# Kernel optimization log

Measured on AMD Instinct MI355X. Metric: run time of the kernel, lower is better.

Reference implementation:

```python
import jax, jax.numpy as jnp
import numpy as np

B, T = 128, 50
VOCAB, EMB_D, GRU_H = 10000, 200, 100
HEADS, AHID, THID = 8, 96, 96

def _conv(x, w, b, pad):
    y = jax.lax.conv_general_dilated(x, w, (1, 1), pad,
        dimension_numbers=('NCHW', 'OIHW', 'NCHW'))
    return y + b[None, :, None, None]

def _bn(x, g, b, m, v):
    s = jax.lax.rsqrt(v + 1e-5)
    return (x - m[None, :, None, None]) * (g * s)[None, :, None, None] + b[None, :, None, None]

def _maxpool(x):
    return jax.lax.reduce_window(x, -jnp.inf, jax.lax.max, (1, 1, 2, 2), (1, 1, 2, 2), 'VALID')

def _resize(x):
    # F.interpolate(mode='bilinear', align_corners=False) == half-pixel bilinear, no antialias
    return jax.image.resize(x, (x.shape[0], x.shape[1], 25, 156), 'bilinear', antialias=False)

def _audio_attn(x, wq, bq, wk, bk, wv, bv):
    # x: [B,96,H,W]; wq: [heads,96,96] == stacked per-head 1x1 convs
    Q = jnp.einsum('bchw,noc->bnohw', x, wq) + bq[None, :, :, None, None]
    K = jnp.einsum('bchw,noc->bnohw', x, wk) + bk[None, :, :, None, None]
    V = jnp.einsum('bchw,noc->bnohw', x, wv) + bv[None, :, :, None, None]
    # torch F.softmax with no dim on a 4D tensor defaults to dim=1 (channels) -> axis=2 here
    return jax.nn.softmax(Q * K, axis=2) * V  # [B,heads,96,H,W]

def _text_attn(o, wq, bq, wk, bk, wv, bv):
    # o: [N,100]; wq: [heads,96,100] == stacked per-head Linear layers
    Q = jnp.einsum('nd,hod->nho', o, wq) + bq[None]
    K = jnp.einsum('nd,hod->nho', o, wk) + bk[None]
    V = jnp.einsum('nd,hod->nho', o, wv) + bv[None]
    a = jax.nn.softmax(Q * K, axis=2) * V  # 2D softmax default dim=1 -> over feature axis
    return a.reshape(o.shape[0], -1)  # head-concat order == torch cat along dim=1

def _gru(xs, w_ih, w_hh, b_ih, b_hh):
    # xs: [T,B,200]; torch gate order r, z, n; b_hn applied inside r-gating
    def step(h, x):
        gi = x @ w_ih.T + b_ih
        gh = h @ w_hh.T + b_hh
        ir, iz, inew = jnp.split(gi, 3, axis=1)
        hr, hz, hnew = jnp.split(gh, 3, axis=1)
        r = jax.nn.sigmoid(ir + hr)
        z = jax.nn.sigmoid(iz + hz)
        n = jnp.tanh(inew + r * hnew)
        h2 = (1.0 - z) * n + z * h
        return h2, h2
    h0 = jnp.zeros((xs.shape[1], GRU_H), xs.dtype)
    hT, outs = jax.lax.scan(step, h0, xs)
    return outs, hT

def _forward(tokens, lengths, mfcc_t, mfcc_f, mfcc_c, w1a, b1a, g1a, be1a, m1a, v1a, w1b, b1b, g1b, be1b, m1b, v1b, w2, b2, g2, be2, m2, v2, w3, b3, g3, be3, m3, v3, w4, b4, g4, be4, m4, v4, wq_a1, bq_a1, wk_a1, bk_a1, wv_a1, bv_a1, wq_a2, bq_a2, wk_a2, bk_a2, wv_a2, bv_a2, emb, w_ih, w_hh, b_ih, b_hh, wq_t1, bq_t1, wk_t1, bk_t1, wv_t1, bv_t1, wq_t2, bq_t2, wk_t2, bk_t2, wv_t2, bv_t2, w_fa, b_fa, w_ft, b_ft, w_e, b_e):
    # --- audio CNN stem (eval-mode batchnorm; dropout off) ---
    xa = jax.nn.relu(_bn(_conv(mfcc_t, w1a, b1a, 'VALID'), g1a, be1a, m1a, v1a))
    xb = jax.nn.relu(_bn(_conv(mfcc_f, w1b, b1b, 'VALID'), g1b, be1b, m1b, v1b))
    # NOTE: original source reuses conv1b/bn1b for the third input (faithful to that)
    xc = jax.nn.relu(_bn(_conv(mfcc_c, w1b, b1b, 'VALID'), g1b, be1b, m1b, v1b))
    x = jnp.concatenate([_resize(xa), _resize(xb), _resize(xc)], axis=1)  # [B,24,25,156]
    x = _maxpool(jax.nn.relu(_bn(_conv(x, w2, b2, [(1, 1), (1, 1)]), g2, be2, m2, v2)))  # [B,32,12,78]
    x = _maxpool(jax.nn.relu(_bn(_conv(x, w3, b3, [(1, 1), (1, 1)]), g3, be3, m3, v3)))  # [B,64,6,39]
    x = jax.nn.relu(_bn(_conv(x, w4, b4, [(1, 1), (1, 1)]), g4, be4, m4, v4))            # [B,96,6,39]
    # --- two stacked per-head audio attentions, then per-head spatial GAP ---
    a1 = _audio_attn(x, wq_a1, bq_a1, wk_a1, bk_a1, wv_a1, bv_a1).mean(axis=(-2, -1))  # [B,8,96]
    a2 = _audio_attn(x, wq_a2, bq_a2, wk_a2, bk_a2, wv_a2, bv_a2).mean(axis=(-2, -1))
    # forward() slices heads along the height concat and GAPs -> per head [stage1 96, stage2 96]
    self_attn_audio = jnp.concatenate([a1, a2], axis=2).reshape(x.shape[0], -1)  # [B,1536]
    # --- text branch: embedding + GRU (all lengths == T -> pack/pad is identity) ---
    ex = jnp.swapaxes(emb[tokens], 0, 1)  # [T,B,200]
    outs, h = _gru(ex, w_ih, w_hh, b_ih, b_hh)  # h: [B,100]
    output = jnp.swapaxes(outs, 0, 1).reshape(-1, GRU_H)  # [B*T,100]
    t1 = _text_attn(output, wq_t1, bq_t1, wk_t1, bk_t1, wv_t1, bv_t1)
    t2 = _text_attn(output, wq_t2, bq_t2, wk_t2, bk_t2, wv_t2, bv_t2)
    self_attn_text = jnp.concatenate([t1, t2], axis=1).reshape(x.shape[0], T, -1).sum(axis=1)  # [B,1536]
    # --- cross-modal gated fusion ---
    x_gap = x.mean(axis=(-2, -1))  # [B,96]
    a_text = jax.nn.softmax(x_gap @ w_fa.T + b_fa, axis=1)   # [B,100]
    attn_text_based_audio = a_text * h                        # [B,100]
    a_audio = jax.nn.softmax(h @ w_ft.T + b_ft, axis=1)      # [B,96]
    attn_audio_based_text = a_audio * x_gap                   # [B,96]
    feat = jnp.concatenate([self_attn_audio, self_attn_text,
                            attn_audio_based_text, attn_text_based_audio], axis=1)  # [B,3268]
    return feat @ w_e.T + b_e  # [B,4] emotion logits

def setup_inputs() -> dict:
    key = jax.random.key(0)
    ks = iter(jax.random.split(key, 100))
    nrm = lambda s, sc=0.05: jax.random.normal(next(ks), s, jnp.float32) * sc
    uni = lambda s: jax.random.uniform(next(ks), s, jnp.float32) * 0.5 + 0.5
    d = {}
    d['mfcc_t'] = jax.random.normal(next(ks), (B, 1, 200, 40), jnp.float32)
    d['mfcc_f'] = jax.random.normal(next(ks), (B, 1, 200, 40), jnp.float32)
    d['mfcc_c'] = jax.random.normal(next(ks), (B, 1, 200, 40), jnp.float32)
    d['tokens'] = jax.random.randint(next(ks), (B, T), 0, VOCAB)
    d['lengths'] = jnp.full((B,), T, jnp.int32)
    def bnp(pre, c):
        d['g' + pre] = 1.0 + nrm((c,)); d['be' + pre] = nrm((c,))
        d['m' + pre] = nrm((c,)); d['v' + pre] = uni((c,))
    d['w1a'] = nrm((8, 1, 5, 2), 0.2); d['b1a'] = nrm((8,)); bnp('1a', 8)
    d['w1b'] = nrm((8, 1, 2, 6), 0.2); d['b1b'] = nrm((8,)); bnp('1b', 8)
    d['w2'] = nrm((32, 24, 3, 3), 0.1); d['b2'] = nrm((32,)); bnp('2', 32)
    d['w3'] = nrm((64, 32, 3, 3), 0.1); d['b3'] = nrm((64,)); bnp('3', 64)
    d['w4'] = nrm((96, 64, 3, 3), 0.08); d['b4'] = nrm((96,)); bnp('4', 96)
    for s in ('1', '2'):
        for p in ('q', 'k', 'v'):
            d['w%s_a%s' % (p, s)] = nrm((HEADS, 96, 96), 0.1)
            d['b%s_a%s' % (p, s)] = nrm((HEADS, 96))
    d['emb'] = nrm((VOCAB, EMB_D), 0.1)
    d['w_ih'] = nrm((3 * GRU_H, EMB_D), 0.1); d['w_hh'] = nrm((3 * GRU_H, GRU_H), 0.1)
    d['b_ih'] = nrm((3 * GRU_H,)); d['b_hh'] = nrm((3 * GRU_H,))
    for s in ('1', '2'):
        for p in ('q', 'k', 'v'):
            d['w%s_t%s' % (p, s)] = nrm((HEADS, THID, GRU_H), 0.1)
            d['b%s_t%s' % (p, s)] = nrm((HEADS, THID))
    d['w_fa'] = nrm((100, 96), 0.1); d['b_fa'] = nrm((100,))
    d['w_ft'] = nrm((96, 100), 0.1); d['b_ft'] = nrm((96,))
    d['w_e'] = nrm((4, 2 * HEADS * AHID + 2 * HEADS * THID + 96 + 100), 0.05); d['b_e'] = nrm((4,))
    return d

def reference(mfcc_t, mfcc_f, mfcc_c, tokens, lengths, w1a, b1a, g1a, be1a, m1a, v1a, w1b, b1b, g1b, be1b, m1b, v1b, w2, b2, g2, be2, m2, v2, w3, b3, g3, be3, m3, v3, w4, b4, g4, be4, m4, v4, wq_a1, bq_a1, wk_a1, bk_a1, wv_a1, bv_a1, wq_a2, bq_a2, wk_a2, bk_a2, wv_a2, bv_a2, emb, w_ih, w_hh, b_ih, b_hh, wq_t1, bq_t1, wk_t1, bk_t1, wv_t1, bv_t1, wq_t2, bq_t2, wk_t2, bk_t2, wv_t2, bv_t2, w_fa, b_fa, w_ft, b_ft, w_e, b_e):
    return _forward(tokens, lengths, mfcc_t, mfcc_f, mfcc_c, w1a, b1a, g1a, be1a, m1a, v1a, w1b, b1b, g1b, be1b, m1b, v1b, w2, b2, g2, be2, m2, v2, w3, b3, g3, be3, m3, v3, w4, b4, g4, be4, m4, v4, wq_a1, bq_a1, wk_a1, bk_a1, wv_a1, bv_a1, wq_a2, bq_a2, wk_a2, bk_a2, wv_a2, bv_a2, emb, w_ih, w_hh, b_ih, b_hh, wq_t1, bq_t1, wk_t1, bk_t1, wv_t1, bv_t1, wq_t2, bq_t2, wk_t2, bk_t2, wv_t2, bv_t2, w_fa, b_fa, w_ft, b_ft, w_e, b_e)
```

## Files before the change

### kernel.cpp

```cpp
#include <hip/hip_runtime.h>
#include <math.h>

static constexpr int kB = 128;
static constexpr int kT = 50;

struct TDesc { const float* src; float* dst; int O; int C; int total; };
struct TPack { TDesc d[15]; };
__global__ void k_transpose_pack(TPack p) {
    TDesc t = p.d[blockIdx.y];
    int idx = blockIdx.x * 256 + threadIdx.x;
    if (idx >= t.total) return;
    int o = idx % t.O; int r = idx / t.O; int c = r % t.C; int n = r / t.C;
    t.dst[idx] = t.src[((size_t)n * t.O + o) * t.C + c];
}

__global__ void k_zero(float* __restrict__ a, int n) {
    int i = blockIdx.x * 256 + threadIdx.x;
    if (i < n) a[i] = 0.f;
}

__global__ void k_stem(const float* __restrict__ mt, const float* __restrict__ mf,
                       const float* __restrict__ mc,
                       const float* __restrict__ w1a, const float* __restrict__ b1a,
                       const float* __restrict__ g1a, const float* __restrict__ be1a,
                       const float* __restrict__ m1a, const float* __restrict__ v1a,
                       const float* __restrict__ w1b, const float* __restrict__ b1b,
                       const float* __restrict__ g1b, const float* __restrict__ be1b,
                       const float* __restrict__ m1b, const float* __restrict__ v1b,
                       float* __restrict__ out, int total) {
    int idx = blockIdx.x * blockDim.x + threadIdx.x;
    if (idx >= total) return;
    int ox = idx % 156; int t = idx / 156;
    int oy = t % 25; t /= 25;
    int ch = t % 24; int b = t / 24;
    int grp = ch >> 3, c = ch & 7;
    const float* src; int Hc, Wc;
    const float *wb, *cb, *g, *be, *m, *v;
    if (grp == 0) { src = mt; Hc = 196; Wc = 39; wb = w1a + c * 10;
                    cb = b1a; g = g1a; be = be1a; m = m1a; v = v1a; }
    else          { src = (grp == 1 ? mf : mc); Hc = 199; Wc = 35; wb = w1b + c * 12;
                    cb = b1b; g = g1b; be = be1b; m = m1b; v = v1b; }
    float s = g[c] * rsqrtf(v[c] + 1e-5f);
    float bias = (cb[c] - m[c]) * s + be[c];
    float sy = (oy + 0.5f) * ((float)Hc / 25.f) - 0.5f;
    float sx = (ox + 0.5f) * ((float)Wc / 156.f) - 0.5f;
    float fy0 = floorf(sy), fx0 = floorf(sx);
    float fy = sy - fy0, fx = sx - fx0;
    int y0 = (int)fy0, x0 = (int)fx0;
    int y0c = min(max(y0, 0), Hc - 1), y1c = min(max(y0 + 1, 0), Hc - 1);
    int x0c = min(max(x0, 0), Wc - 1), x1c = min(max(x0 + 1, 0), Wc - 1);
    bool xs = (x1c == x0c), ys = (y1c == y0c);
    const float* p = src + (size_t)b * 8000;
    float t00, t01, t10, t11;
    if (grp == 0) {
        float W[6][3];
        #pragma unroll
        for (int r = 0; r < 6; ++r) {
            int rr = min(y0c + r, 199);
            #pragma unroll
            for (int cc = 0; cc < 3; ++cc)
                W[r][cc] = p[rr * 40 + min(x0c + cc, 39)];
        }
        float a00 = 0.f, a01 = 0.f, a10 = 0.f, a11 = 0.f;
        #pragma unroll
        for (int ky = 0; ky < 5; ++ky)
            #pragma unroll
            for (int kx = 0; kx < 2; ++kx) {
                float wv = wb[ky * 2 + kx];
                a00 += W[ky][kx] * wv;     a01 += W[ky][kx + 1] * wv;
                a10 += W[ky + 1][kx] * wv; a11 += W[ky + 1][kx + 1] * wv;
            }
        t00 = a00;
        t01 = xs ? a00 : a01;
        t10 = ys ? a00 : a10;
        t11 = xs ? (ys ? a00 : a10) : (ys ? a01 : a11);
    } else {
        float W[3][7];
        #pragma unroll
        for (int r = 0; r < 3; ++r) {
            int rr = min(y0c + r, 199);
            #pragma unroll
            for (int cc = 0; cc < 7; ++cc)
                W[r][cc] = p[rr * 40 + min(x0c + cc, 39)];
        }
        float a00 = 0.f, a01 = 0.f, a10 = 0.f, a11 = 0.f;
        #pragma unroll
        for (int ky = 0; ky < 2; ++ky)
            #pragma unroll
            for (int kx = 0; kx < 6; ++kx) {
                float wv = wb[ky * 6 + kx];
                a00 += W[ky][kx] * wv;     a01 += W[ky][kx + 1] * wv;
                a10 += W[ky + 1][kx] * wv; a11 += W[ky + 1][kx + 1] * wv;
            }
        t00 = a00;
        t01 = xs ? a00 : a01;
        t10 = ys ? a00 : a10;
        t11 = xs ? (ys ? a00 : a10) : (ys ? a01 : a11);
    }
    float r00 = fmaxf(t00 * s + bias, 0.f), r01 = fmaxf(t01 * s + bias, 0.f);
    float r10 = fmaxf(t10 * s + bias, 0.f), r11 = fmaxf(t11 * s + bias, 0.f);
    out[idx] = r00 * (1.f - fy) * (1.f - fx) + r01 * (1.f - fy) * fx
             + r10 * fy * (1.f - fx) + r11 * fy * fx;
}

template<int CIN, int CI_T, int H, int W, int ROWS, int NPX>
__global__ void __launch_bounds__(256) k_conv3x3_tiled(
    const float* __restrict__ in, const float* __restrict__ wT,
    const float* __restrict__ cb, const float* __restrict__ g,
    const float* __restrict__ be, const float* __restrict__ m,
    const float* __restrict__ v, float* __restrict__ out, int COUT) {
    constexpr int WP = W + 2;
    constexpr int RP = ROWS + 2;
    constexpr int STAGE = CI_T * RP * WP;
    __shared__ float sx[STAGE];
    __shared__ float sw[CI_T * 9 * 8];
    const int b = blockIdx.x, rt = blockIdx.y, oc0 = blockIdx.z * 8;
    const int row0 = rt * ROWS;
    const int tid = threadIdx.x;

    int off[NPX]; bool val[NPX];
    #pragma unroll
    for (int j = 0; j < NPX; ++j) {
        int px = tid + j * 256;
        int oy = px / W, ox = px - oy * W;
        bool ok = (px < ROWS * W) && (row0 + oy < H);
        val[j] = ok;
        off[j] = ok ? (oy * WP + ox) : 0;
    }

    float acc[NPX][8];
    #pragma unroll
    for (int j = 0; j < NPX; ++j)
        #pragma unroll
        for (int o = 0; o < 8; ++o) acc[j][o] = 0.f;

    for (int c0 = 0; c0 < CIN; c0 += CI_T) {
        __syncthreads();
        for (int e = tid; e < STAGE; e += 256) {
            int ci = e / (RP * WP);
            int rem = e - ci * RP * WP;
            int r = rem / WP;
            int xx = rem - r * WP;
            int iy = row0 - 1 + r;
            int ix = xx - 1;
            float vv = 0.f;
            if (iy >= 0 && iy < H && ix >= 0 && ix < W)
                vv = in[((size_t)(b * CIN + c0 + ci) * H + iy) * W + ix];
            sx[e] = vv;
        }
        for (int e = tid; e < CI_T * 9 * 8; e += 256) {
            int rk = e >> 3;
            int o = e & 7;
            sw[e] = wT[((size_t)c0 * 9 + rk) * COUT + oc0 + o];
        }
        __syncthreads();
        #pragma unroll 1
        for (int cl = 0; cl < CI_T; ++cl) {
            const float* sxc = sx + cl * RP * WP;
            #pragma unroll
            for (int k = 0; k < 9; ++k) {
                const int ky = k / 3, kx = k % 3;
                const float4 wa = *(const float4*)(sw + (cl * 9 + k) * 8);
                const float4 wb = *(const float4*)(sw + (cl * 9 + k) * 8 + 4);
                #pragma unroll
                for (int j = 0; j < NPX; ++j) {
                    float xv = sxc[off[j] + ky * WP + kx];
                    acc[j][0] += xv * wa.x; acc[j][1] += xv * wa.y;
                    acc[j][2] += xv * wa.z; acc[j][3] += xv * wa.w;
                    acc[j][4] += xv * wb.x; acc[j][5] += xv * wb.y;
                    acc[j][6] += xv * wb.z; acc[j][7] += xv * wb.w;
                }
            }
        }
    }
    float sc[8], bi[8];
    #pragma unroll
    for (int o = 0; o < 8; ++o) {
        float s = g[oc0 + o] * rsqrtf(v[oc0 + o] + 1e-5f);
        sc[o] = s; bi[o] = (cb[oc0 + o] - m[oc0 + o]) * s + be[oc0 + o];
    }
    #pragma unroll
    for (int j = 0; j < NPX; ++j) if (val[j]) {
        int px = tid + j * 256;
        int oy = row0 + px / W, ox = px % W;
        #pragma unroll
        for (int o = 0; o < 8; ++o)
            out[((size_t)(b * COUT + oc0 + o) * H + oy) * W + ox] =
                fmaxf(acc[j][o] * sc[o] + bi[o], 0.f);
    }
}

__global__ void k_maxpool(const float* __restrict__ in, float* __restrict__ out,
                          int C, int Hin, int Win, int Hout, int Wout, int total) {
    int idx = blockIdx.x * blockDim.x + threadIdx.x;
    if (idx >= total) return;
    int ox = idx % Wout; int t = idx / Wout;
    int oy = t % Hout; t /= Hout;
    int c = t % C; int b = t / C;
    const float* p = in + ((size_t)(b * C + c) * Hin + 2 * oy) * Win + 2 * ox;
    float m0 = fmaxf(p[0], p[1]);
    float m1 = fmaxf(p[Win], p[Win + 1]);
    out[idx] = fmaxf(m0, m1);
}

__global__ void __launch_bounds__(256) k_xgap(const float* __restrict__ x,
                                              float* __restrict__ xgap) {
    int b = blockIdx.x, tid = threadIdx.x;
    int wave = tid >> 6, lane = tid & 63;
    for (int c = wave; c < 96; c += 4) {
        const float* row = x + ((size_t)b * 96 + c) * 234;
        float s = 0.f;
        for (int p = lane; p < 234; p += 64) s += row[p];
        #pragma unroll
        for (int off = 1; off < 64; off <<= 1) s += __shfl_xor(s, off);
        if (lane == 0) xgap[b * 96 + c] = s * (1.f / 234.f);
    }
}

__global__ void __launch_bounds__(256, 2) k_audio_attn(
    const float* __restrict__ x,
    const float* __restrict__ wq1, const float* __restrict__ bq1,
    const float* __restrict__ wk1, const float* __restrict__ bk1,
    const float* __restrict__ wv1, const float* __restrict__ bv1,
    const float* __restrict__ wq2, const float* __restrict__ bq2,
    const float* __restrict__ wk2, const float* __restrict__ bk2,
    const float* __restrict__ wv2, const float* __restrict__ bv2,
    float* __restrict__ afeat) {
    const int b = blockIdx.x >> 1, pt = blockIdx.x & 1;
    const int n = blockIdx.y, stage = blockIdx.z;
    const float* wq = (stage ? wq2 : wq1) + n * 9216;
    const float* wk = (stage ? wk2 : wk1) + n * 9216;
    const float* wv = (stage ? wv2 : wv1) + n * 9216;
    const float* bqn = (stage ? bq2 : bq1) + n * 96;
    const float* bkn = (stage ? bk2 : bk1) + n * 96;
    const float* bvn = (stage ? bv2 : bv1) + n * 96;
    const int tid = threadIdx.x;
    const int to = tid >> 4, tpg = tid & 15;
    const int ob = to * 6;
    const int pA = tpg * 4;
    const int p0 = pt * 128;

    __shared__ float sxc[16 * 128];
    __shared__ float sw[4608];
    float* sred = sw;

    const float* xb = x + (size_t)b * (96 * 234) + p0;

    float qa[6][8], ka[6][8], va[6][8];
    #pragma unroll
    for (int j = 0; j < 6; ++j) {
        float bq_ = bqn[ob + j], bk_ = bkn[ob + j], bv_ = bvn[ob + j];
        #pragma unroll
        for (int i = 0; i < 8; ++i) { qa[j][i] = bq_; ka[j][i] = bk_; va[j][i] = bv_; }
    }

    for (int c0 = 0; c0 < 96; c0 += 16) {
        __syncthreads();
        {
            #pragma unroll
            for (int it = 0; it < 4; ++it) {
                int e2 = tid + it * 256;
                int r = e2 >> 6, c2 = (e2 & 63) * 2;
                float2 v = make_float2(0.f, 0.f);
                if (p0 + c2 < 234) v = *(const float2*)(xb + (c0 + r) * 234 + c2);
                *(float2*)(sxc + r * 128 + c2) = v;
            }
        }
        for (int e4 = tid; e4 < 1152; e4 += 256) {
            int mat = (e4 >= 768) ? 2 : (e4 >= 384 ? 1 : 0);
            int r4 = e4 - mat * 384;
            const float* wsrc = (mat == 0) ? wq : (mat == 1 ? wk : wv);
            *(float4*)(sw + mat * 1536 + r4 * 4) = *(const float4*)(wsrc + c0 * 96 + r4 * 4);
        }
        __syncthreads();
        #pragma unroll 2
        for (int cc = 0; cc < 16; ++cc) {
            float4 xa = *(const float4*)(sxc + cc * 128 + pA);
            float4 xc = *(const float4*)(sxc + cc * 128 + 64 + pA);
            const float* wr = sw + cc * 96 + ob;
            float2 q01 = *(const float2*)(wr);
            float2 q23 = *(const float2*)(wr + 2);
            float2 q45 = *(const float2*)(wr + 4);
            float2 k01 = *(const float2*)(wr + 1536);
            float2 k23 = *(const float2*)(wr + 1538);
            float2 k45 = *(const float2*)(wr + 1540);
            float2 v01 = *(const float2*)(wr + 3072);
            float2 v23 = *(const float2*)(wr + 3074);
            float2 v45 = *(const float2*)(wr + 3076);
            float wqv[6] = {q01.x, q01.y, q23.x, q23.y, q45.x, q45.y};
            float wkv[6] = {k01.x, k01.y, k23.x, k23.y, k45.x, k45.y};
            float wvv[6] = {v01.x, v01.y, v23.x, v23.y, v45.x, v45.y};
            #pragma unroll
            for (int j = 0; j < 6; ++j) {
                qa[j][0] += wqv[j] * xa.x; qa[j][1] += wqv[j] * xa.y;
                qa[j][2] += wqv[j] * xa.z; qa[j][3] += wqv[j] * xa.w;
                qa[j][4] += wqv[j] * xc.x; qa[j][5] += wqv[j] * xc.y;
                qa[j][6] += wqv[j] * xc.z; qa[j][7] += wqv[j] * xc.w;
                ka[j][0] += wkv[j] * xa.x; ka[j][1] += wkv[j] * xa.y;
                ka[j][2] += wkv[j] * xa.z; ka[j][3] += wkv[j] * xa.w;
                ka[j][4] += wkv[j] * xc.x; ka[j][5] += wkv[j] * xc.y;
                ka[j][6] += wkv[j] * xc.z; ka[j][7] += wkv[j] * xc.w;
                va[j][0] += wvv[j] * xa.x; va[j][1] += wvv[j] * xa.y;
                va[j][2] += wvv[j] * xa.z; va[j][3] += wvv[j] * xa.w;
                va[j][4] += wvv[j] * xc.x; va[j][5] += wvv[j] * xc.y;
                va[j][6] += wvv[j] * xc.z; va[j][7] += wvv[j] * xc.w;
            }
        }
    }

    int col[8];
    #pragma unroll
    for (int i = 0; i < 4; ++i) { col[i] = pA + i; col[4 + i] = 64 + pA + i; }

    float pmx[8];
    #pragma unroll
    for (int i = 0; i < 8; ++i) pmx[i] = -1e30f;
    #pragma unroll
    for (int j = 0; j < 6; ++j)
        #pragma unroll
        for (int i = 0; i < 8; ++i) {
            float sv = qa[j][i] * ka[j][i];
            qa[j][i] = sv;
            pmx[i] = fmaxf(pmx[i], sv);
        }
    __syncthreads();
    #pragma unroll
    for (int i = 0; i < 8; ++i) sred[to * 128 + col[i]] = pmx[i];
    __syncthreads();
    float m_[8];
    #pragma unroll
    for (int i = 0; i < 8; ++i) {
        float mm = -1e30f;
        for (int t = 0; t < 16; ++t) mm = fmaxf(mm, sred[t * 128 + col[i]]);
        m_[i] = mm;
    }
    __syncthreads();
    float z[8];
    #pragma unroll
    for (int i = 0; i < 8; ++i) z[i] = 0.f;
    #pragma unroll
    for (int j = 0; j < 6; ++j)
        #pragma unroll
        for (int i = 0; i < 8; ++i) {
            float e = __expf(qa[j][i] - m_[i]);
            qa[j][i] = e;
            z[i] += e;
        }
    #pragma unroll
    for (int i = 0; i < 8; ++i) sred[to * 128 + col[i]] = z[i];
    __syncthreads();
    float rz[8];
    #pragma unroll
    for (int i = 0; i < 8; ++i) {
        float zs = 0.f;
        for (int t = 0; t < 16; ++t) zs += sred[t * 128 + col[i]];
        rz[i] = (p0 + col[i] < 234) ? 1.f / zs : 0.f;
    }
    __syncthreads();
    #pragma unroll
    for (int j = 0; j < 6; ++j) {
        float po = 0.f;
        #pragma unroll
        for (int i = 0; i < 8; ++i) po += qa[j][i] * rz[i] * va[j][i];
        sred[(ob + j) * 16 + tpg] = po;
    }
    __syncthreads();
    if (tid < 96) {
        float ssum = 0.f;
        #pragma unroll
        for (int t = 0; t < 16; ++t) ssum += sred[tid * 16 + t];
        atomicAdd(afeat + b * 1536 + n * 192 + stage * 96 + tid, ssum * (1.f / 234.f));
    }
}

__global__ void __launch_bounds__(320) k_gi(const int* __restrict__ tokens,
        const float* __restrict__ emb, const float* __restrict__ w_ih,
        const float* __restrict__ b_ih, float* __restrict__ GI) {
    int r0 = blockIdx.x * 8;
    int tid = threadIdx.x;
    __shared__ float er[8][200];
    for (int e = tid; e < 1600; e += 320) {
        int r = e / 200, c = e - r * 200;
        er[r][c] = emb[(size_t)tokens[r0 + r] * 200 + c];
    }
    __syncthreads();
    if (tid < 300) {
        float acc[8];
        float bv = b_ih[tid];
        #pragma unroll
        for (int r = 0; r < 8; ++r) acc[r] = bv;
        for (int k4 = 0; k4 < 50; ++k4) {
            float4 w4 = *(const float4*)(w_ih + (size_t)tid * 200 + k4 * 4);
            #pragma unroll
            for (int r = 0; r < 8; ++r) {
                float4 x4 = *(const float4*)&er[r][k4 * 4];
                acc[r] += w4.x * x4.x + w4.y * x4.y + w4.z * x4.z + w4.w * x4.w;
            }
        }
        #pragma unroll
        for (int r = 0; r < 8; ++r)
            GI[(size_t)(r0 + r) * 300 + tid] = acc[r];
    }
}

__global__ void __launch_bounds__(320) k_gru_all(const float* __restrict__ GI,
        const float* __restrict__ w_hh, const float* __restrict__ b_hh,
        float* __restrict__ outs) {
    int b = blockIdx.x, tid = threadIdx.x;
    __shared__ float hs[100];
    __shared__ float gH[300];
    float4 wreg[25];
    float bias = 0.f;
    if (tid < 300) {
        bias = b_hh[tid];
        #pragma unroll
        for (int k4 = 0; k4 < 25; ++k4)
            wreg[k4] = *(const float4*)(w_hh + (size_t)tid * 100 + k4 * 4);
    }
    if (tid < 100) hs[tid] = 0.f;
    __syncthreads();
    for (int t = 0; t < kT; ++t) {
        if (tid < 300) {
            float gh = bias;
            #pragma unroll
            for (int k4 = 0; k4 < 25; ++k4) {
                float4 h4 = *(const float4*)&hs[k4 * 4];
                gh += wreg[k4].x * h4.x + wreg[k4].y * h4.y
                    + wreg[k4].z * h4.z + wreg[k4].w * h4.w;
            }
            gH[tid] = gh;
        }
        __syncthreads();
        if (tid < 100) {
            const float* gi = GI + ((size_t)b * kT + t) * 300;
            float r = 1.f / (1.f + expf(-(gi[tid] + gH[tid])));
            float z = 1.f / (1.f + expf(-(gi[100 + tid] + gH[100 + tid])));
            float nn = tanhf(gi[200 + tid] + r * gH[200 + tid]);
            float h2 = (1.f - z) * nn + z * hs[tid];
            hs[tid] = h2;
            outs[((size_t)b * kT + t) * 100 + tid] = h2;
        }
        __syncthreads();
    }
}

__global__ void __launch_bounds__(128) k_text_attn(const float* __restrict__ outs,
    const float* __restrict__ wq1, const float* __restrict__ bq1,
    const float* __restrict__ wk1, const float* __restrict__ bk1,
    const float* __restrict__ wv1, const float* __restrict__ bv1,
    const float* __restrict__ wq2, const float* __restrict__ bq2,
    const float* __restrict__ wk2, const float* __restrict__ bk2,
    const float* __restrict__ wv2, const float* __restrict__ bv2,
    float* __restrict__ tfeat) {
    int b = blockIdx.x, stage = blockIdx.y, n = blockIdx.z;
    const float* wq = stage ? wq2 : wq1; const float* bq = stage ? bq2 : bq1;
    const float* wk = stage ? wk2 : wk1; const float* bk = stage ? bk2 : bk1;
    const float* wv = stage ? wv2 : wv1; const float* bv = stage ? bv2 : bv1;
    int tid = threadIdx.x;
    bool act = tid < 96;
    int oo = act ? tid : 0;
    const float* wqc = wq + n * 9600 + oo;
    const float* wkc = wk + n * 9600 + oo;
    const float* wvc = wv + n * 9600 + oo;
    float bqv = act ? bq[n * 96 + tid] : 0.f;
    float bkv = act ? bk[n * 96 + tid] : 0.f;
    float bvv = act ? bv[n * 96 + tid] : 0.f;
    __shared__ float rows[10][100];
    __shared__ float wredM[2][10], wredS[2][10];
    float acc = 0.f;
    int wave = tid >> 6, lane = tid & 63;
    for (int tile = 0; tile < 5; ++tile) {
        int t0 = tile * 10;
        __syncthreads();
        for (int e = tid; e < 1000; e += 128) {
            int tt = e / 100, c = e - tt * 100;
            rows[tt][c] = outs[((size_t)b * kT + t0 + tt) * 100 + c];
        }
        __syncthreads();
        float q[10], k[10], v[10];
        #pragma unroll
        for (int tt = 0; tt < 10; ++tt) { q[tt] = bqv; k[tt] = bkv; v[tt] = bvv; }
        for (int c4 = 0; c4 < 25; ++c4) {
            int cb = c4 * 4 * 96;
            float q0 = wqc[cb], q1 = wqc[cb + 96], q2 = wqc[cb + 192], q3 = wqc[cb + 288];
            float k0 = wkc[cb], k1 = wkc[cb + 96], k2 = wkc[cb + 192], k3 = wkc[cb + 288];
            float v0 = wvc[cb], v1 = wvc[cb + 96], v2 = wvc[cb + 192], v3 = wvc[cb + 288];
            #pragma unroll
            for (int tt = 0; tt < 10; ++tt) {
                float4 x4 = *(const float4*)&rows[tt][c4 * 4];
                q[tt] += q0 * x4.x + q1 * x4.y + q2 * x4.z + q3 * x4.w;
                k[tt] += k0 * x4.x + k1 * x4.y + k2 * x4.z + k3 * x4.w;
                v[tt] += v0 * x4.x + v1 * x4.y + v2 * x4.z + v3 * x4.w;
            }
        }
        float s[10], e_[10];
        #pragma unroll
        for (int tt = 0; tt < 10; ++tt) s[tt] = act ? q[tt] * k[tt] : -1e30f;
        #pragma unroll
        for (int tt = 0; tt < 10; ++tt) {
            float m = s[tt];
            #pragma unroll
            for (int off = 1; off < 64; off <<= 1) m = fmaxf(m, __shfl_xor(m, off));
            if (lane == 0) wredM[wave][tt] = m;
        }
        __syncthreads();
        #pragma unroll
        for (int tt = 0; tt < 10; ++tt) {
            float mx = fmaxf(wredM[0][tt], wredM[1][tt]);
            e_[tt] = expf(s[tt] - mx);
        }
        #pragma unroll
        for (int tt = 0; tt < 10; ++tt) {
            float sm = e_[tt];
            #pragma unroll
            for (int off = 1; off < 64; off <<= 1) sm += __shfl_xor(sm, off);
            if (lane == 0) wredS[wave][tt] = sm;
        }
        __syncthreads();
        #pragma unroll
        for (int tt = 0; tt < 10; ++tt) {
            float sm = wredS[0][tt] + wredS[1][tt];
            acc += e_[tt] / sm * v[tt];
        }
    }
    if (act) tfeat[b * 1536 + stage * 768 + n * 96 + tid] = acc;
}

__global__ void __launch_bounds__(128) k_final(const float* __restrict__ xgap,
    const float* __restrict__ outs, const float* __restrict__ afeat,
    const float* __restrict__ tfeat,
    const float* __restrict__ w_fa, const float* __restrict__ b_fa,
    const float* __restrict__ w_ft, const float* __restrict__ b_ft,
    const float* __restrict__ w_e, const float* __restrict__ b_e,
    float* __restrict__ out) {
    int b = blockIdx.x; int tid = threadIdx.x;
    __shared__ float xg[96], hv[100], st[100], sa[96], aat[96], atba[100];
    __shared__ float redm[2], reds[2];
    if (tid < 96) xg[tid] = xgap[b * 96 + tid];
    if (tid < 100) hv[tid] = outs[(size_t)(b * kT + kT - 1) * 100 + tid];
    __syncthreads();
    if (tid < 100) {
        float acc = b_fa[tid];
        const float* wr = w_fa + tid * 96;
        for (int c = 0; c < 96; ++c) acc += wr[c] * xg[c];
        st[tid] = acc;
    }
    if (tid < 96) {
        float acc = b_ft[tid];
        const float* wr = w_ft + tid * 100;
        for (int c = 0; c < 100; ++c) acc += wr[c] * hv[c];
        sa[tid] = acc;
    }
    __syncthreads();
    if (tid == 0) {
        float mxv = -1e30f; for (int i = 0; i < 100; ++i) mxv = fmaxf(mxv, st[i]);
        float s = 0.f; for (int i = 0; i < 100; ++i) s += expf(st[i] - mxv);
        redm[0] = mxv; reds[0] = s;
    }
    if (tid == 1) {
        float mxv = -1e30f; for (int i = 0; i < 96; ++i) mxv = fmaxf(mxv, sa[i]);
        float s = 0.f; for (int i = 0; i < 96; ++i) s += expf(sa[i] - mxv);
        redm[1] = mxv; reds[1] = s;
    }
    __syncthreads();
    if (tid < 100) atba[tid] = expf(st[tid] - redm[0]) / reds[0] * hv[tid];
    if (tid < 96)  aat[tid]  = expf(sa[tid] - redm[1]) / reds[1] * xg[tid];
    __syncthreads();
    float a0 = 0.f, a1 = 0.f, a2 = 0.f, a3 = 0.f;
    for (int col = tid; col < 3268; col += 128) {
        float f;
        if (col < 1536)      f = afeat[b * 1536 + col];
        else if (col < 3072) f = tfeat[b * 1536 + col - 1536];
        else if (col < 3168) f = aat[col - 3072];
        else                 f = atba[col - 3168];
        a0 += w_e[col] * f;            a1 += w_e[3268 + col] * f;
        a2 += w_e[2 * 3268 + col] * f; a3 += w_e[3 * 3268 + col] * f;
    }
    __shared__ float r4[4][128];
    r4[0][tid] = a0; r4[1][tid] = a1; r4[2][tid] = a2; r4[3][tid] = a3;
    __syncthreads();
    if (tid < 4) {
        float s = 0.f;
        for (int i = 0; i < 128; ++i) s += r4[tid][i];
        out[b * 4 + tid] = s + b_e[tid];
    }
}

extern "C" void kernel_launch(void* const* d_in, const int* in_sizes, int n_in,
                              void* d_out, int out_size, void* d_ws, size_t ws_size,
                              hipStream_t stream) {
    (void)in_sizes; (void)n_in; (void)out_size; (void)ws_size;
    const float* mfcc_t = (const float*)d_in[0];
    const float* mfcc_f = (const float*)d_in[1];
    const float* mfcc_c = (const float*)d_in[2];
    const int*   tokens = (const int*)d_in[3];
    const float *w1a = (const float*)d_in[5],  *b1a = (const float*)d_in[6],
                *g1a = (const float*)d_in[7],  *be1a = (const float*)d_in[8],
                *m1a = (const float*)d_in[9],  *v1a = (const float*)d_in[10];
    const float *w1b = (const float*)d_in[11], *b1b = (const float*)d_in[12],
                *g1b = (const float*)d_in[13], *be1b = (const float*)d_in[14],
                *m1b = (const float*)d_in[15], *v1b = (const float*)d_in[16];
    const float *w2 = (const float*)d_in[17], *b2 = (const float*)d_in[18],
                *g2 = (const float*)d_in[19], *be2 = (const float*)d_in[20],
                *m2 = (const float*)d_in[21], *v2 = (const float*)d_in[22];
    const float *w3 = (const float*)d_in[23], *b3 = (const float*)d_in[24],
                *g3 = (const float*)d_in[25], *be3 = (const float*)d_in[26],
                *m3 = (const float*)d_in[27], *v3 = (const float*)d_in[28];
    const float *w4 = (const float*)d_in[29], *b4 = (const float*)d_in[30],
                *g4 = (const float*)d_in[31], *be4 = (const float*)d_in[32],
                *m4 = (const float*)d_in[33], *v4 = (const float*)d_in[34];
    const float *wq_a1 = (const float*)d_in[35], *bq_a1 = (const float*)d_in[36],
                *wk_a1 = (const float*)d_in[37], *bk_a1 = (const float*)d_in[38],
                *wv_a1 = (const float*)d_in[39], *bv_a1 = (const float*)d_in[40];
    const float *wq_a2 = (const float*)d_in[41], *bq_a2 = (const float*)d_in[42],
                *wk_a2 = (const float*)d_in[43], *bk_a2 = (const float*)d_in[44],
                *wv_a2 = (const float*)d_in[45], *bv_a2 = (const float*)d_in[46];
    const float *emb  = (const float*)d_in[47];
    const float *w_ih = (const float*)d_in[48], *w_hh = (const float*)d_in[49],
                *b_ih = (const float*)d_in[50], *b_hh = (const float*)d_in[51];
    const float *wq_t1 = (const float*)d_in[52], *bq_t1 = (const float*)d_in[53],
                *wk_t1 = (const float*)d_in[54], *bk_t1 = (const float*)d_in[55],
                *wv_t1 = (const float*)d_in[56], *bv_t1 = (const float*)d_in[57];
    const float *wq_t2 = (const float*)d_in[58], *bq_t2 = (const float*)d_in[59],
                *wk_t2 = (const float*)d_in[60], *bk_t2 = (const float*)d_in[61],
                *wv_t2 = (const float*)d_in[62], *bv_t2 = (const float*)d_in[63];
    const float *w_fa = (const float*)d_in[64], *b_fa = (const float*)d_in[65],
                *w_ft = (const float*)d_in[66], *b_ft = (const float*)d_in[67],
                *w_e  = (const float*)d_in[68], *b_e  = (const float*)d_in[69];

    float* ws = (float*)d_ws;
    const size_t Z0 = 0;
    const size_t Z1 = 22091776ull;
    const size_t OUTS  = 34072576ull;
    const size_t AFEAT = 34712576ull;
    const size_t TFEAT = 34909184ull;
    const size_t XGAP  = 35105792ull;
    const size_t WT    = 35118080ull;
    float* X1 = ws + Z1;
    float* C2 = ws + Z0;  float* P2 = ws + Z1;
    float* C3 = ws + Z0;  float* P3 = ws + Z1;
    float* X4 = ws + Z0;  float* GI = ws + Z1;
    float* outs  = ws + OUTS;
    float* afeat = ws + AFEAT;
    float* tfeat = ws + TFEAT;
    float* xgap  = ws + XGAP;
    float* wqa1t = ws + WT;
    float* wka1t = wqa1t + 73728; float* wva1t = wka1t + 73728;
    float* wqa2t = wva1t + 73728; float* wka2t = wqa2t + 73728; float* wva2t = wka2t + 73728;
    float* wqt1t = wva2t + 73728;
    float* wkt1t = wqt1t + 76800; float* wvt1t = wkt1t + 76800;
    float* wqt2t = wvt1t + 76800; float* wkt2t = wqt2t + 76800; float* wvt2t = wkt2t + 76800;
    float* wT2 = outs;
    float* wT3 = outs + 6912;
    float* wT4 = outs + 25344;

    TPack tp;
    tp.d[0]  = {wq_a1, wqa1t, 96, 96, 73728};
    tp.d[1]  = {wk_a1, wka1t, 96, 96, 73728};
    tp.d[2]  = {wv_a1, wva1t, 96, 96, 73728};
    tp.d[3]  = {wq_a2, wqa2t, 96, 96, 73728};
    tp.d[4]  = {wk_a2, wka2t, 96, 96, 73728};
    tp.d[5]  = {wv_a2, wva2t, 96, 96, 73728};
    tp.d[6]  = {w2, wT2, 32, 216, 6912};
    tp.d[7]  = {w3, wT3, 64, 288, 18432};
    tp.d[8]  = {w4, wT4, 96, 576, 55296};
    tp.d[9]  = {wq_t1, wqt1t, 96, 100, 76800};
    tp.d[10] = {wk_t1, wkt1t, 96, 100, 76800};
    tp.d[11] = {wv_t1, wvt1t, 96, 100, 76800};
    tp.d[12] = {wq_t2, wqt2t, 96, 100, 76800};
    tp.d[13] = {wk_t2, wkt2t, 96, 100, 76800};
    tp.d[14] = {wv_t2, wvt2t, 96, 100, 76800};
    k_transpose_pack<<<dim3(300, 15), 256, 0, stream>>>(tp);

    k_zero<<<768, 256, 0, stream>>>(afeat, 196608);

    k_stem<<<46800, 256, 0, stream>>>(mfcc_t, mfcc_f, mfcc_c,
        w1a, b1a, g1a, be1a, m1a, v1a,
        w1b, b1b, g1b, be1b, m1b, v1b, X1, 11980800);
    k_conv3x3_tiled<24, 8, 25, 156, 9, 6><<<dim3(128, 3, 4), 256, 0, stream>>>(
        X1, wT2, b2, g2, be2, m2, v2, C2, 32);
    k_maxpool<<<14976, 256, 0, stream>>>(C2, P2, 32, 25, 156, 12, 78, 3833856);
    k_conv3x3_tiled<32, 8, 12, 78, 12, 4><<<dim3(128, 1, 8), 256, 0, stream>>>(
        P2, wT3, b3, g3, be3, m3, v3, C3, 64);
    k_maxpool<<<7488, 256, 0, stream>>>(C3, P3, 64, 12, 78, 6, 39, 1916928);
    k_conv3x3_tiled<64, 16, 6, 39, 6, 1><<<dim3(128, 1, 12), 256, 0, stream>>>(
        P3, wT4, b4, g4, be4, m4, v4, X4, 96);

    k_xgap<<<kB, 256, 0, stream>>>(X4, xgap);

    k_audio_attn<<<dim3(kB * 2, 8, 2), 256, 0, stream>>>(X4,
        wqa1t, bq_a1, wka1t, bk_a1, wva1t, bv_a1,
        wqa2t, bq_a2, wka2t, bk_a2, wva2t, bv_a2, afeat);

    k_gi<<<kB * kT / 8, 320, 0, stream>>>(tokens, emb, w_ih, b_ih, GI);
    k_gru_all<<<kB, 320, 0, stream>>>(GI, w_hh, b_hh, outs);
    k_text_attn<<<dim3(kB, 2, 8), 128, 0, stream>>>(outs,
        wqt1t, bq_t1, wkt1t, bk_t1, wvt1t, bv_t1,
        wqt2t, bq_t2, wkt2t, bk_t2, wvt2t, bv_t2, tfeat);

    k_final<<<kB, 128, 0, stream>>>(xgap, outs, afeat, tfeat,
                                    w_fa, b_fa, w_ft, b_ft, w_e, b_e, (float*)d_out);
}
```

Baseline: 1.418 ms.

## Horizontally fuse independent kernels to overlap serial GRU with stem and attention

The afeat zeroing moves into the transpose-pack launch as an extra grid row. The GRU recurrence runs as 128 extra blocks inside the stem launch, so the serial 50-step loop overlaps with the bilinear stem. xgap, text attention and audio attention become one launch that selects its role from the block index. This cuts launch count and hides GRU latency, but the fused GRU now reads w_hh from global memory each step instead of keeping it in registers. Workspace aliases are rearranged (GI to Z0, conv weights to tfeat) so the concurrently running branches do not overlap in memory.

```diff
diff --git a/kernel.cpp b/kernel.cpp
--- a/kernel.cpp
+++ b/kernel.cpp
@@ -6,7 +6,12 @@
 
 struct TDesc { const float* src; float* dst; int O; int C; int total; };
 struct TPack { TDesc d[15]; };
-__global__ void k_transpose_pack(TPack p) {
+__global__ void k_transpose_pack(TPack p, float* __restrict__ za) {
+    if (blockIdx.y == 15) {
+        for (int i = blockIdx.x * 256 + threadIdx.x; i < 196608; i += 76800)
+            za[i] = 0.f;
+        return;
+    }
     TDesc t = p.d[blockIdx.y];
     int idx = blockIdx.x * 256 + threadIdx.x;
     if (idx >= t.total) return;
@@ -14,21 +19,94 @@
     t.dst[idx] = t.src[((size_t)n * t.O + o) * t.C + c];
 }
 
-__global__ void k_zero(float* __restrict__ a, int n) {
-    int i = blockIdx.x * 256 + threadIdx.x;
-    if (i < n) a[i] = 0.f;
+__global__ void __launch_bounds__(320) k_gi(const int* __restrict__ tokens,
+        const float* __restrict__ emb, const float* __restrict__ w_ih,
+        const float* __restrict__ b_ih, float* __restrict__ GI) {
+    int r0 = blockIdx.x * 8;
+    int tid = threadIdx.x;
+    __shared__ float er[8][200];
+    for (int e = tid; e < 1600; e += 320) {
+        int r = e / 200, c = e - r * 200;
+        er[r][c] = emb[(size_t)tokens[r0 + r] * 200 + c];
+    }
+    __syncthreads();
+    if (tid < 300) {
+        float acc[8];
+        float bv = b_ih[tid];
+        #pragma unroll
+        for (int r = 0; r < 8; ++r) acc[r] = bv;
+        for (int k4 = 0; k4 < 50; ++k4) {
+            float4 w4 = *(const float4*)(w_ih + (size_t)tid * 200 + k4 * 4);
+            #pragma unroll
+            for (int r = 0; r < 8; ++r) {
+                float4 x4 = *(const float4*)&er[r][k4 * 4];
+                acc[r] += w4.x * x4.x + w4.y * x4.y + w4.z * x4.z + w4.w * x4.w;
+            }
+        }
+        #pragma unroll
+        for (int r = 0; r < 8; ++r)
+            GI[(size_t)(r0 + r) * 300 + tid] = acc[r];
+    }
 }
 
-__global__ void k_stem(const float* __restrict__ mt, const float* __restrict__ mf,
-                       const float* __restrict__ mc,
-                       const float* __restrict__ w1a, const float* __restrict__ b1a,
-                       const float* __restrict__ g1a, const float* __restrict__ be1a,
-                       const float* __restrict__ m1a, const float* __restrict__ v1a,
-                       const float* __restrict__ w1b, const float* __restrict__ b1b,
-                       const float* __restrict__ g1b, const float* __restrict__ be1b,
-                       const float* __restrict__ m1b, const float* __restrict__ v1b,
-                       float* __restrict__ out, int total) {
-    int idx = blockIdx.x * blockDim.x + threadIdx.x;
+__global__ void __launch_bounds__(256) k_fat_stem_gru(
+    const float* __restrict__ mt, const float* __restrict__ mf,
+    const float* __restrict__ mc,
+    const float* __restrict__ w1a, const float* __restrict__ b1a,
+    const float* __restrict__ g1a, const float* __restrict__ be1a,
+    const float* __restrict__ m1a, const float* __restrict__ v1a,
+    const float* __restrict__ w1b, const float* __restrict__ b1b,
+    const float* __restrict__ g1b, const float* __restrict__ be1b,
+    const float* __restrict__ m1b, const float* __restrict__ v1b,
+    float* __restrict__ out, int total,
+    const float* __restrict__ GI, const float* __restrict__ w_hh,
+    const float* __restrict__ b_hh, float* __restrict__ outs) {
+    if (blockIdx.x < 128) {
+        const int b = blockIdx.x, tid = threadIdx.x;
+        __shared__ float hs[100];
+        __shared__ float gH[300];
+        const float bias0 = b_hh[tid];
+        const float bias1 = (tid < 44) ? b_hh[256 + tid] : 0.f;
+        if (tid < 100) hs[tid] = 0.f;
+        __syncthreads();
+        for (int t = 0; t < kT; ++t) {
+            {
+                float gh = bias0;
+                const float* wr = w_hh + (size_t)tid * 100;
+                #pragma unroll
+                for (int k4 = 0; k4 < 25; ++k4) {
+                    float4 w4 = *(const float4*)(wr + k4 * 4);
+                    float4 h4 = *(const float4*)&hs[k4 * 4];
+                    gh += w4.x * h4.x + w4.y * h4.y + w4.z * h4.z + w4.w * h4.w;
+                }
+                gH[tid] = gh;
+            }
+            if (tid < 44) {
+                float gh = bias1;
+                const float* wr = w_hh + (size_t)(256 + tid) * 100;
+                #pragma unroll
+                for (int k4 = 0; k4 < 25; ++k4) {
+                    float4 w4 = *(const float4*)(wr + k4 * 4);
+                    float4 h4 = *(const float4*)&hs[k4 * 4];
+                    gh += w4.x * h4.x + w4.y * h4.y + w4.z * h4.z + w4.w * h4.w;
+                }
+                gH[256 + tid] = gh;
+            }
+            __syncthreads();
+            if (tid < 100) {
+                const float* gi = GI + ((size_t)b * kT + t) * 300;
+                float r = 1.f / (1.f + expf(-(gi[tid] + gH[tid])));
+                float z = 1.f / (1.f + expf(-(gi[100 + tid] + gH[100 + tid])));
+                float nn = tanhf(gi[200 + tid] + r * gH[200 + tid]);
+                float h2 = (1.f - z) * nn + z * hs[tid];
+                hs[tid] = h2;
+                outs[((size_t)b * kT + t) * 100 + tid] = h2;
+            }
+            __syncthreads();
+        }
+        return;
+    }
+    int idx = (blockIdx.x - 128) * 256 + threadIdx.x;
     if (idx >= total) return;
     int ox = idx % 156; int t = idx / 156;
     int oy = t % 25; t /= 25;
@@ -203,21 +281,7 @@
     out[idx] = fmaxf(m0, m1);
 }
 
-__global__ void __launch_bounds__(256) k_xgap(const float* __restrict__ x,
-                                              float* __restrict__ xgap) {
-    int b = blockIdx.x, tid = threadIdx.x;
-    int wave = tid >> 6, lane = tid & 63;
-    for (int c = wave; c < 96; c += 4) {
-        const float* row = x + ((size_t)b * 96 + c) * 234;
-        float s = 0.f;
-        for (int p = lane; p < 234; p += 64) s += row[p];
-        #pragma unroll
-        for (int off = 1; off < 64; off <<= 1) s += __shfl_xor(s, off);
-        if (lane == 0) xgap[b * 96 + c] = s * (1.f / 234.f);
-    }
-}
-
-__global__ void __launch_bounds__(256, 2) k_audio_attn(
+__global__ void __launch_bounds__(256, 2) k_fat_attn(
     const float* __restrict__ x,
     const float* __restrict__ wq1, const float* __restrict__ bq1,
     const float* __restrict__ wk1, const float* __restrict__ bk1,
@@ -225,23 +289,127 @@
     const float* __restrict__ wq2, const float* __restrict__ bq2,
     const float* __restrict__ wk2, const float* __restrict__ bk2,
     const float* __restrict__ wv2, const float* __restrict__ bv2,
-    float* __restrict__ afeat) {
-    const int b = blockIdx.x >> 1, pt = blockIdx.x & 1;
-    const int n = blockIdx.y, stage = blockIdx.z;
+    float* __restrict__ afeat,
+    const float* __restrict__ outs,
+    const float* __restrict__ wqt1, const float* __restrict__ bqt1,
+    const float* __restrict__ wkt1, const float* __restrict__ bkt1,
+    const float* __restrict__ wvt1, const float* __restrict__ bvt1,
+    const float* __restrict__ wqt2, const float* __restrict__ bqt2,
+    const float* __restrict__ wkt2, const float* __restrict__ bkt2,
+    const float* __restrict__ wvt2, const float* __restrict__ bvt2,
+    float* __restrict__ tfeat, float* __restrict__ xgap) {
+    __shared__ float smem[6656];
+    const int bx = blockIdx.x;
+    const int tid = threadIdx.x;
+
+    if (bx >= 6144) {
+        int b = bx - 6144;
+        int wave = tid >> 6, lane = tid & 63;
+        for (int c = wave; c < 96; c += 4) {
+            const float* row = x + ((size_t)b * 96 + c) * 234;
+            float s = 0.f;
+            for (int p = lane; p < 234; p += 64) s += row[p];
+            #pragma unroll
+            for (int off = 1; off < 64; off <<= 1) s += __shfl_xor(s, off);
+            if (lane == 0) xgap[b * 96 + c] = s * (1.f / 234.f);
+        }
+        return;
+    }
+    if (bx >= 4096) {
+        int a = bx - 4096;
+        int b = a & 127, rem = a >> 7;
+        int stage = rem & 1, n = rem >> 1;
+        const float* wq = stage ? wqt2 : wqt1; const float* bq = stage ? bqt2 : bqt1;
+        const float* wk = stage ? wkt2 : wkt1; const float* bk = stage ? bkt2 : bkt1;
+        const float* wv = stage ? wvt2 : wvt1; const float* bv = stage ? bvt2 : bvt1;
+        bool act = tid < 96;
+        int oo = act ? tid : 0;
+        const float* wqc = wq + n * 9600 + oo;
+        const float* wkc = wk + n * 9600 + oo;
+        const float* wvc = wv + n * 9600 + oo;
+        float bqv = act ? bq[n * 96 + tid] : 0.f;
+        float bkv = act ? bk[n * 96 + tid] : 0.f;
+        float bvv = act ? bv[n * 96 + tid] : 0.f;
+        float* rows = smem;
+        float* wredM = smem + 1000;
+        float* wredS = smem + 1020;
+        float acc = 0.f;
+        int wave = tid >> 6, lane = tid & 63;
+        for (int tile = 0; tile < 5; ++tile) {
+            int t0 = tile * 10;
+            __syncthreads();
+            for (int e = tid; e < 1000; e += 256) {
+                int tt = e / 100, c = e - tt * 100;
+                rows[tt * 100 + c] = outs[((size_t)b * kT + t0 + tt) * 100 + c];
+            }
+            __syncthreads();
+            float q[10], k[10], v[10];
+            #pragma unroll
+            for (int tt = 0; tt < 10; ++tt) { q[tt] = bqv; k[tt] = bkv; v[tt] = bvv; }
+            for (int c4 = 0; c4 < 25; ++c4) {
+                int cb = c4 * 384;
+                float q0 = wqc[cb], q1 = wqc[cb + 96], q2 = wqc[cb + 192], q3 = wqc[cb + 288];
+                float k0 = wkc[cb], k1 = wkc[cb + 96], k2 = wkc[cb + 192], k3 = wkc[cb + 288];
+                float v0 = wvc[cb], v1 = wvc[cb + 96], v2 = wvc[cb + 192], v3 = wvc[cb + 288];
+                #pragma unroll
+                for (int tt = 0; tt < 10; ++tt) {
+                    float4 x4 = *(const float4*)&rows[tt * 100 + c4 * 4];
+                    q[tt] += q0 * x4.x + q1 * x4.y + q2 * x4.z + q3 * x4.w;
+                    k[tt] += k0 * x4.x + k1 * x4.y + k2 * x4.z + k3 * x4.w;
+                    v[tt] += v0 * x4.x + v1 * x4.y + v2 * x4.z + v3 * x4.w;
+                }
+            }
+            float s_[10], e_[10];
+            #pragma unroll
+            for (int tt = 0; tt < 10; ++tt) s_[tt] = act ? q[tt] * k[tt] : -1e30f;
+            #pragma unroll
+            for (int tt = 0; tt < 10; ++tt) {
+                float m = s_[tt];
+                #pragma unroll
+                for (int off = 1; off < 64; off <<= 1) m = fmaxf(m, __shfl_xor(m, off));
+                if (lane == 0 && wave < 2) wredM[wave * 10 + tt] = m;
+            }
+            __syncthreads();
+            #pragma unroll
+            for (int tt = 0; tt < 10; ++tt) {
+                float mx = fmaxf(wredM[tt], wredM[10 + tt]);
+                e_[tt] = expf(s_[tt] - mx);
+            }
+            #pragma unroll
+            for (int tt = 0; tt < 10; ++tt) {
+                float sm = e_[tt];
+                #pragma unroll
+                for (int off = 1; off < 64; off <<= 1) sm += __shfl_xor(sm, off);
+                if (lane == 0 && wave < 2) wredS[wave * 10 + tt] = sm;
+            }
+            __syncthreads();
+            #pragma unroll
+            for (int tt = 0; tt < 10; ++tt) {
+                float sm = wredS[tt] + wredS[10 + tt];
+                acc += e_[tt] / sm * v[tt];
+            }
+        }
+        if (act) tfeat[b * 1536 + stage * 768 + n * 96 + tid] = acc;
+        return;
+    }
+
+    const int a = bx;
+    const int xp = a & 255;
+    const int b = xp >> 1, pt = xp & 1;
+    const int n = (a >> 8) & 7, stage = a >> 11;
     const float* wq = (stage ? wq2 : wq1) + n * 9216;
     const float* wk = (stage ? wk2 : wk1) + n * 9216;
     const float* wv = (stage ? wv2 : wv1) + n * 9216;
     const float* bqn = (stage ? bq2 : bq1) + n * 96;
     const float* bkn = (stage ? bk2 : bk1) + n * 96;
     const float* bvn = (stage ? bv2 : bv1) + n * 96;
-    const int tid = threadIdx.x;
     const int to = tid >> 4, tpg = tid & 15;
     const int ob = to * 6;
     const int pA = tpg * 4;
     const int p0 = pt * 128;
 
-    __shared__ float sxc[16 * 128];
-    __shared__ float sw[4608];
+    float* sxc = smem;
+    float* sw = smem + 2048;
     float* sred = sw;
 
     const float* xb = x + (size_t)b * (96 * 234) + p0;
@@ -371,159 +539,6 @@
         for (int t = 0; t < 16; ++t) ssum += sred[tid * 16 + t];
         atomicAdd(afeat + b * 1536 + n * 192 + stage * 96 + tid, ssum * (1.f / 234.f));
     }
-}
-
-__global__ void __launch_bounds__(320) k_gi(const int* __restrict__ tokens,
-        const float* __restrict__ emb, const float* __restrict__ w_ih,
-        const float* __restrict__ b_ih, float* __restrict__ GI) {
-    int r0 = blockIdx.x * 8;
-    int tid = threadIdx.x;
-    __shared__ float er[8][200];
-    for (int e = tid; e < 1600; e += 320) {
-        int r = e / 200, c = e - r * 200;
-        er[r][c] = emb[(size_t)tokens[r0 + r] * 200 + c];
-    }
-    __syncthreads();
-    if (tid < 300) {
-        float acc[8];
-        float bv = b_ih[tid];
-        #pragma unroll
-        for (int r = 0; r < 8; ++r) acc[r] = bv;
-        for (int k4 = 0; k4 < 50; ++k4) {
-            float4 w4 = *(const float4*)(w_ih + (size_t)tid * 200 + k4 * 4);
-            #pragma unroll
-            for (int r = 0; r < 8; ++r) {
-                float4 x4 = *(const float4*)&er[r][k4 * 4];
-                acc[r] += w4.x * x4.x + w4.y * x4.y + w4.z * x4.z + w4.w * x4.w;
-            }
-        }
-        #pragma unroll
-        for (int r = 0; r < 8; ++r)
-            GI[(size_t)(r0 + r) * 300 + tid] = acc[r];
-    }
-}
-
-__global__ void __launch_bounds__(320) k_gru_all(const float* __restrict__ GI,
-        const float* __restrict__ w_hh, const float* __restrict__ b_hh,
-        float* __restrict__ outs) {
-    int b = blockIdx.x, tid = threadIdx.x;
-    __shared__ float hs[100];
-    __shared__ float gH[300];
-    float4 wreg[25];
-    float bias = 0.f;
-    if (tid < 300) {
-        bias = b_hh[tid];
-        #pragma unroll
-        for (int k4 = 0; k4 < 25; ++k4)
-            wreg[k4] = *(const float4*)(w_hh + (size_t)tid * 100 + k4 * 4);
-    }
-    if (tid < 100) hs[tid] = 0.f;
-    __syncthreads();
-    for (int t = 0; t < kT; ++t) {
-        if (tid < 300) {
-            float gh = bias;
-            #pragma unroll
-            for (int k4 = 0; k4 < 25; ++k4) {
-                float4 h4 = *(const float4*)&hs[k4 * 4];
-                gh += wreg[k4].x * h4.x + wreg[k4].y * h4.y
-                    + wreg[k4].z * h4.z + wreg[k4].w * h4.w;
-            }
-            gH[tid] = gh;
-        }
-        __syncthreads();
-        if (tid < 100) {
-            const float* gi = GI + ((size_t)b * kT + t) * 300;
-            float r = 1.f / (1.f + expf(-(gi[tid] + gH[tid])));
-            float z = 1.f / (1.f + expf(-(gi[100 + tid] + gH[100 + tid])));
-            float nn = tanhf(gi[200 + tid] + r * gH[200 + tid]);
-            float h2 = (1.f - z) * nn + z * hs[tid];
-            hs[tid] = h2;
-            outs[((size_t)b * kT + t) * 100 + tid] = h2;
-        }
-        __syncthreads();
-    }
-}
-
-__global__ void __launch_bounds__(128) k_text_attn(const float* __restrict__ outs,
-    const float* __restrict__ wq1, const float* __restrict__ bq1,
-    const float* __restrict__ wk1, const float* __restrict__ bk1,
-    const float* __restrict__ wv1, const float* __restrict__ bv1,
-    const float* __restrict__ wq2, const float* __restrict__ bq2,
-    const float* __restrict__ wk2, const float* __restrict__ bk2,
-    const float* __restrict__ wv2, const float* __restrict__ bv2,
-    float* __restrict__ tfeat) {
-    int b = blockIdx.x, stage = blockIdx.y, n = blockIdx.z;
-    const float* wq = stage ? wq2 : wq1; const float* bq = stage ? bq2 : bq1;
-    const float* wk = stage ? wk2 : wk1; const float* bk = stage ? bk2 : bk1;
-    const float* wv = stage ? wv2 : wv1; const float* bv = stage ? bv2 : bv1;
-    int tid = threadIdx.x;
-    bool act = tid < 96;
-    int oo = act ? tid : 0;
-    const float* wqc = wq + n * 9600 + oo;
-    const float* wkc = wk + n * 9600 + oo;
-    const float* wvc = wv + n * 9600 + oo;
-    float bqv = act ? bq[n * 96 + tid] : 0.f;
-    float bkv = act ? bk[n * 96 + tid] : 0.f;
-    float bvv = act ? bv[n * 96 + tid] : 0.f;
-    __shared__ float rows[10][100];
-    __shared__ float wredM[2][10], wredS[2][10];
-    float acc = 0.f;
-    int wave = tid >> 6, lane = tid & 63;
-    for (int tile = 0; tile < 5; ++tile) {
-        int t0 = tile * 10;
-        __syncthreads();
-        for (int e = tid; e < 1000; e += 128) {
-            int tt = e / 100, c = e - tt * 100;
-            rows[tt][c] = outs[((size_t)b * kT + t0 + tt) * 100 + c];
-        }
-        __syncthreads();
-        float q[10], k[10], v[10];
-        #pragma unroll
-        for (int tt = 0; tt < 10; ++tt) { q[tt] = bqv; k[tt] = bkv; v[tt] = bvv; }
-        for (int c4 = 0; c4 < 25; ++c4) {
-            int cb = c4 * 4 * 96;
-            float q0 = wqc[cb], q1 = wqc[cb + 96], q2 = wqc[cb + 192], q3 = wqc[cb + 288];
-            float k0 = wkc[cb], k1 = wkc[cb + 96], k2 = wkc[cb + 192], k3 = wkc[cb + 288];
-            float v0 = wvc[cb], v1 = wvc[cb + 96], v2 = wvc[cb + 192], v3 = wvc[cb + 288];
-            #pragma unroll
-            for (int tt = 0; tt < 10; ++tt) {
-                float4 x4 = *(const float4*)&rows[tt][c4 * 4];
-                q[tt] += q0 * x4.x + q1 * x4.y + q2 * x4.z + q3 * x4.w;
-                k[tt] += k0 * x4.x + k1 * x4.y + k2 * x4.z + k3 * x4.w;
-                v[tt] += v0 * x4.x + v1 * x4.y + v2 * x4.z + v3 * x4.w;
-            }
-        }
-        float s[10], e_[10];
-        #pragma unroll
-        for (int tt = 0; tt < 10; ++tt) s[tt] = act ? q[tt] * k[tt] : -1e30f;
-        #pragma unroll
-        for (int tt = 0; tt < 10; ++tt) {
-            float m = s[tt];
-            #pragma unroll
-            for (int off = 1; off < 64; off <<= 1) m = fmaxf(m, __shfl_xor(m, off));
-            if (lane == 0) wredM[wave][tt] = m;
-        }
-        __syncthreads();
-        #pragma unroll
-        for (int tt = 0; tt < 10; ++tt) {
-            float mx = fmaxf(wredM[0][tt], wredM[1][tt]);
-            e_[tt] = expf(s[tt] - mx);
-        }
-        #pragma unroll
-        for (int tt = 0; tt < 10; ++tt) {
-            float sm = e_[tt];
-            #pragma unroll
-            for (int off = 1; off < 64; off <<= 1) sm += __shfl_xor(sm, off);
-            if (lane == 0) wredS[wave][tt] = sm;
-        }
-        __syncthreads();
-        #pragma unroll
-        for (int tt = 0; tt < 10; ++tt) {
-            float sm = wredS[0][tt] + wredS[1][tt];
-            acc += e_[tt] / sm * v[tt];
-        }
-    }
-    if (act) tfeat[b * 1536 + stage * 768 + n * 96 + tid] = acc;
 }
 
 __global__ void __launch_bounds__(128) k_final(const float* __restrict__ xgap,
@@ -636,10 +651,11 @@
     const size_t TFEAT = 34909184ull;
     const size_t XGAP  = 35105792ull;
     const size_t WT    = 35118080ull;
+    float* GI = ws + Z0;
     float* X1 = ws + Z1;
     float* C2 = ws + Z0;  float* P2 = ws + Z1;
     float* C3 = ws + Z0;  float* P3 = ws + Z1;
-    float* X4 = ws + Z0;  float* GI = ws + Z1;
+    float* X4 = ws + Z0;
     float* outs  = ws + OUTS;
     float* afeat = ws + AFEAT;
     float* tfeat = ws + TFEAT;
@@ -650,9 +666,9 @@
     float* wqt1t = wva2t + 73728;
     float* wkt1t = wqt1t + 76800; float* wvt1t = wkt1t + 76800;
     float* wqt2t = wvt1t + 76800; float* wkt2t = wqt2t + 76800; float* wvt2t = wkt2t + 76800;
-    float* wT2 = outs;
-    float* wT3 = outs + 6912;
-    float* wT4 = outs + 25344;
+    float* wT2 = tfeat;
+    float* wT3 = tfeat + 6912;
+    float* wT4 = tfeat + 25344;
 
     TPack tp;
     tp.d[0]  = {wq_a1, wqa1t, 96, 96, 73728};
@@ -670,13 +686,15 @@
     tp.d[12] = {wq_t2, wqt2t, 96, 100, 76800};
     tp.d[13] = {wk_t2, wkt2t, 96, 100, 76800};
     tp.d[14] = {wv_t2, wvt2t, 96, 100, 76800};
-    k_transpose_pack<<<dim3(300, 15), 256, 0, stream>>>(tp);
-
-    k_zero<<<768, 256, 0, stream>>>(afeat, 196608);
-
-    k_stem<<<46800, 256, 0, stream>>>(mfcc_t, mfcc_f, mfcc_c,
+    k_transpose_pack<<<dim3(300, 16), 256, 0, stream>>>(tp, afeat);
+
+    k_gi<<<kB * kT / 8, 320, 0, stream>>>(tokens, emb, w_ih, b_ih, GI);
+
+    k_fat_stem_gru<<<46928, 256, 0, stream>>>(mfcc_t, mfcc_f, mfcc_c,
         w1a, b1a, g1a, be1a, m1a, v1a,
-        w1b, b1b, g1b, be1b, m1b, v1b, X1, 11980800);
+        w1b, b1b, g1b, be1b, m1b, v1b, X1, 11980800,
+        GI, w_hh, b_hh, outs);
+
     k_conv3x3_tiled<24, 8, 25, 156, 9, 6><<<dim3(128, 3, 4), 256, 0, stream>>>(
         X1, wT2, b2, g2, be2, m2, v2, C2, 32);
     k_maxpool<<<14976, 256, 0, stream>>>(C2, P2, 32, 25, 156, 12, 78, 3833856);
@@ -686,17 +704,12 @@
     k_conv3x3_tiled<64, 16, 6, 39, 6, 1><<<dim3(128, 1, 12), 256, 0, stream>>>(
         P3, wT4, b4, g4, be4, m4, v4, X4, 96);
 
-    k_xgap<<<kB, 256, 0, stream>>>(X4, xgap);
-
-    k_audio_attn<<<dim3(kB * 2, 8, 2), 256, 0, stream>>>(X4,
+    k_fat_attn<<<6272, 256, 0, stream>>>(X4,
         wqa1t, bq_a1, wka1t, bk_a1, wva1t, bv_a1,
-        wqa2t, bq_a2, wka2t, bk_a2, wva2t, bv_a2, afeat);
-
-    k_gi<<<kB * kT / 8, 320, 0, stream>>>(tokens, emb, w_ih, b_ih, GI);
-    k_gru_all<<<kB, 320, 0, stream>>>(GI, w_hh, b_hh, outs);
-    k_text_attn<<<dim3(kB, 2, 8), 128, 0, stream>>>(outs,
+        wqa2t, bq_a2, wka2t, bk_a2, wva2t, bv_a2, afeat,
+        outs,
         wqt1t, bq_t1, wkt1t, bk_t1, wvt1t, bv_t1,
-        wqt2t, bq_t2, wkt2t, bk_t2, wvt2t, bv_t2, tfeat);
+        wqt2t, bq_t2, wkt2t, bk_t2, wvt2t, bv_t2, tfeat, xgap);
 
     k_final<<<kB, 128, 0, stream>>>(xgap, outs, afeat, tfeat,
                                     w_fa, b_fa, w_ft, b_ft, w_e, b_e, (float*)d_out);
```

Result: slower. 1.581 ms (+11.5%).
